# Kernel tuning notes

Hardware: AMD Instinct MI355X
Metric: run time of the kernel (lower is better)

Reference implementation:

```python
import jax, jax.numpy as jnp
import numpy as np

B, S, D = 1, 2048, 2048
HQ, HKV, HD = 32, 8, 64
EXPAND = HQ // HKV

def _rotate_half(x):
    x1, x2 = x[..., : x.shape[-1] // 2], x[..., x.shape[-1] // 2 :]
    return jnp.concatenate((-x2, x1), axis=-1)

def setup_inputs() -> dict:
    key = jax.random.key(0)
    k1, k2, k3 = jax.random.split(key, 3)
    hidden_states = jax.random.normal(k1, (B, S, D), dtype=jnp.float32)
    # Llama weight init scale ~ small
    Wq = jax.random.normal(k2, (HQ * HD, D), dtype=jnp.float32) * 0.02
    Wk = jax.random.normal(k3, (HKV * HD, D), dtype=jnp.float32) * 0.02
    # true rotary cos/sin tables, shape [B, S, HD]
    inv_freq = 1.0 / (10000.0 ** (jnp.arange(0, HD, 2, dtype=jnp.float32) / HD))
    pos = jnp.arange(S, dtype=jnp.float32)
    freqs = pos[:, None] * inv_freq[None, :]            # [S, HD/2]
    emb = jnp.concatenate((freqs, freqs), axis=-1)       # [S, HD]
    cos = jnp.broadcast_to(jnp.cos(emb)[None], (B, S, HD))
    sin = jnp.broadcast_to(jnp.sin(emb)[None], (B, S, HD))
    attn_mask = jnp.zeros((B, 1, S, S), dtype=jnp.float32)  # accepted but unused by the module
    return {"hidden_states": hidden_states, "cos": cos, "sin": sin,
            "attn_mask": attn_mask, "Wq": Wq, "Wk": Wk}

def reference(hidden_states, cos, sin, attn_mask, Wq, Wk):
    b, s, _ = hidden_states.shape
    # projections (nn.Linear, no bias): x @ W.T
    q = hidden_states @ Wq.T                              # [b, s, HQ*HD]
    k = hidden_states @ Wk.T                              # [b, s, HKV*HD]
    q = q.reshape(b, s, HQ, HD).transpose(0, 2, 1, 3)     # [b, HQ, s, HD]
    k = k.reshape(b, s, HKV, HD).transpose(0, 2, 1, 3)    # [b, HKV, s, HD]
    c = cos[:, None, :, :]                                # unsqueeze_dim=1
    sn = sin[:, None, :, :]
    q = q * c + _rotate_half(q) * sn
    k = k * c + _rotate_half(k) * sn
    k = jnp.repeat(k, EXPAND, axis=1)                     # GQA repeat_interleave -> [b, HQ, s, HD]
    scores = jnp.einsum('bhqd,bhkd->bhqk', q, k)          # NO 1/sqrt(d) scaling (faithful)
    return jax.nn.softmax(scores, axis=-1)
```

## Files before the change

kernel.cpp:

```cpp
#include <hip/hip_runtime.h>
#include <hip/hip_bf16.h>

typedef _Float16 half8 __attribute__((ext_vector_type(8)));
typedef float floatx4 __attribute__((ext_vector_type(4)));

#define SEQ 2048
#define DIM 2048
#define HQ 32
#define HKV 8
#define HD 64
#define NQ (HQ*HD)
#define NK (HKV*HD)
#define NTOT (NQ+NK)
#define LOG2E 1.44269504088896340736f

#define GLOAD_LDS16(g, l) \
    __builtin_amdgcn_global_load_lds( \
        (const __attribute__((address_space(1))) void*)(g), \
        (__attribute__((address_space(3))) void*)(l), 16, 0, 0)

__global__ __launch_bounds__(256) void convert_kernel(
    const float* __restrict__ X, const float* __restrict__ Wq,
    const float* __restrict__ Wk, _Float16* __restrict__ Xh,
    _Float16* __restrict__ Wh)
{
    const long c   = (long)blockIdx.x * 256 + threadIdx.x;
    const long nxc = (long)SEQ * DIM / 8;
    const float* src;
    _Float16* dst;
    if (c < nxc) {
        src = X + c * 8;
        dst = Xh + c * 8;
    } else {
        long f = (c - nxc) * 8;
        src = (f < (long)NQ * DIM) ? Wq + f : Wk + (f - (long)NQ * DIM);
        dst = Wh + f;
    }
    float4 a = ((const float4*)src)[0];
    float4 b = ((const float4*)src)[1];
    half8 h = {(_Float16)a.x, (_Float16)a.y, (_Float16)a.z, (_Float16)a.w,
               (_Float16)b.x, (_Float16)b.y, (_Float16)b.z, (_Float16)b.w};
    *(half8*)dst = h;
}

__global__ __launch_bounds__(256) void gemm1_kernel(
    const _Float16* __restrict__ Xh, const _Float16* __restrict__ Wh,
    const float* __restrict__ cosb, const float* __restrict__ sinb,
    _Float16* __restrict__ qout, _Float16* __restrict__ kout)
{
    __shared__ __align__(16) _Float16 lsA[128 * 64];
    __shared__ __align__(16) _Float16 lsB[128 * 64];
    const int tid  = threadIdx.x;
    const int lane = tid & 63;
    const int wv   = tid >> 6;
    const int wm   = wv & 1, wn = wv >> 1;
    const int m    = lane & 15, quad = lane >> 4;
    const int s0   = blockIdx.x * 128;
    const int n0   = blockIdx.y * 128;

    floatx4 acc[4][4];
    #pragma unroll
    for (int i = 0; i < 4; i++)
        #pragma unroll
        for (int j = 0; j < 4; j++)
            acc[i][j] = floatx4{0.f, 0.f, 0.f, 0.f};

    for (int k0 = 0; k0 < DIM; k0 += 64) {
        __syncthreads();
        #pragma unroll
        for (int r = 0; r < 4; r++) {
            int c    = r * 256 + tid;
            int row  = c >> 3;
            int chg  = (c & 7) ^ (row & 7);
            GLOAD_LDS16(Xh + (long)(s0 + row) * DIM + k0 + chg * 8,
                        (char*)lsA + (r * 256 + wv * 64) * 16);
        }
        #pragma unroll
        for (int r = 0; r < 4; r++) {
            int c    = r * 256 + tid;
            int row  = c >> 3;
            int chg  = (c & 7) ^ (row & 7);
            GLOAD_LDS16(Wh + (long)(n0 + row) * DIM + k0 + chg * 8,
                        (char*)lsB + (r * 256 + wv * 64) * 16);
        }
        __syncthreads();

        #pragma unroll
        for (int kk = 0; kk < 2; kk++) {
            half8 aF[4], bF[4];
            const int pc = ((kk << 2) | quad) ^ (m & 7);
            #pragma unroll
            for (int i = 0; i < 4; i++)
                aF[i] = *(const half8*)(lsA + (wm * 64 + i * 16 + m) * 64 + pc * 8);
            #pragma unroll
            for (int j = 0; j < 4; j++)
                bF[j] = *(const half8*)(lsB + (wn * 64 + j * 16 + m) * 64 + pc * 8);
            #pragma unroll
            for (int i = 0; i < 4; i++)
                #pragma unroll
                for (int j = 0; j < 4; j++)
                    acc[i][j] = __builtin_amdgcn_mfma_f32_16x16x32_f16(
                        aF[i], bF[j], acc[i][j], 0, 0, 0);
        }
    }

    #pragma unroll
    for (int i = 0; i < 4; i++) {
        #pragma unroll
        for (int reg = 0; reg < 4; reg++) {
            int s = s0 + wm * 64 + i * 16 + quad * 4 + reg;
            #pragma unroll
            for (int j = 0; j < 4; j++) {
                int col = n0 + wn * 64 + j * 16 + m;
                int d   = j * 16 + m;
                float v = acc[i][j][reg];
                float partner = (j < 2) ? -acc[i][j + 2][reg] : acc[i][j - 2][reg];
                float cs = cosb[s * HD + d];
                float sn = sinb[s * HD + d];
                float o  = v * cs + partner * sn;
                if (col < NQ) {
                    int hq = col >> 6;
                    qout[((long)hq * SEQ + s) * HD + d] = (_Float16)(o * LOG2E);
                } else {
                    int hk = (col - NQ) >> 6;
                    kout[((long)hk * SEQ + s) * HD + d] = (_Float16)o;
                }
            }
        }
    }
}

__global__ __launch_bounds__(512) void attn_kernel(
    const _Float16* __restrict__ qf, const _Float16* __restrict__ kf,
    float* __restrict__ out)
{
    __shared__ float redm[8][16];
    __shared__ float redl[8][16];
    const int tid  = threadIdx.x;
    const int lane = tid & 63;
    const int w    = tid >> 6;
    const int m    = lane & 15, quad = lane >> 4;
    const int qb   = blockIdx.x;
    const int h    = blockIdx.y;
    const int kvh  = h >> 2;
    const int s0   = qb * 16;

    const _Float16* qbase = qf + ((long)h * SEQ + s0) * HD;
    const _Float16* kbase = kf + (long)kvh * SEQ * HD;

    half8 bQ0 = *(const half8*)(qbase + (long)m * HD + quad * 8);
    half8 bQ1 = *(const half8*)(qbase + (long)m * HD + 32 + quad * 8);

    floatx4 acc[16];
    const _Float16* kp = kbase + (long)(w * 256 + m) * HD + quad * 8;
    half8 aK0 = *(const half8*)(kp);
    half8 aK1 = *(const half8*)(kp + 32);
    #pragma unroll
    for (int ct = 0; ct < 16; ct++) {
        half8 nK0, nK1;
        if (ct < 15) {
            const _Float16* np = kbase + (long)(w * 256 + (ct + 1) * 16 + m) * HD + quad * 8;
            nK0 = *(const half8*)(np);
            nK1 = *(const half8*)(np + 32);
        }
        floatx4 a = floatx4{0.f, 0.f, 0.f, 0.f};
        a = __builtin_amdgcn_mfma_f32_16x16x32_f16(aK0, bQ0, a, 0, 0, 0);
        a = __builtin_amdgcn_mfma_f32_16x16x32_f16(aK1, bQ1, a, 0, 0, 0);
        acc[ct] = a;
        aK0 = nK0;
        aK1 = nK1;
    }

    float lm = acc[0][0];
    #pragma unroll
    for (int ct = 0; ct < 16; ct++)
        #pragma unroll
        for (int r = 0; r < 4; r++) lm = fmaxf(lm, acc[ct][r]);
    lm = fmaxf(lm, __shfl_xor(lm, 16));
    lm = fmaxf(lm, __shfl_xor(lm, 32));
    if (quad == 0) redm[w][m] = lm;
    __syncthreads();
    float g = redm[0][m];
    #pragma unroll
    for (int ww = 1; ww < 8; ww++) g = fmaxf(g, redm[ww][m]);

    float ls = 0.f;
    #pragma unroll
    for (int ct = 0; ct < 16; ct++) {
        #pragma unroll
        for (int r = 0; r < 4; r++) {
            float e = exp2f(acc[ct][r] - g);
            acc[ct][r] = e;
            ls += e;
        }
    }
    ls += __shfl_xor(ls, 16);
    ls += __shfl_xor(ls, 32);
    if (quad == 0) redl[w][m] = ls;
    __syncthreads();
    float tot = 0.f;
    #pragma unroll
    for (int ww = 0; ww < 8; ww++) tot += redl[ww][m];
    float inv = 1.0f / tot;

    float* obase = out + ((long)h * SEQ + s0 + m) * SEQ + w * 256 + quad * 4;
    #pragma unroll
    for (int ct = 0; ct < 16; ct++) {
        floatx4 v = acc[ct];
        v[0] *= inv; v[1] *= inv; v[2] *= inv; v[3] *= inv;
        *(floatx4*)(obase + ct * 16) = v;
    }
}

extern "C" void kernel_launch(void* const* d_in, const int* in_sizes, int n_in,
                              void* d_out, int out_size, void* d_ws, size_t ws_size,
                              hipStream_t stream) {
    const float* hidden = (const float*)d_in[0];
    const float* cosb   = (const float*)d_in[1];
    const float* sinb   = (const float*)d_in[2];
    const float* Wq     = (const float*)d_in[4];
    const float* Wk     = (const float*)d_in[5];
    float* out = (float*)d_out;

    char* ws = (char*)d_ws;
    _Float16* Xh = (_Float16*)ws;
    _Float16* Wh = (_Float16*)(ws + 8388608);
    _Float16* qf = (_Float16*)(ws + 8388608 + 10485760);
    _Float16* kf = (_Float16*)(ws + 8388608 + 10485760 + 8388608);

    convert_kernel<<<4608, 256, 0, stream>>>(hidden, Wq, Wk, Xh, Wh);
    gemm1_kernel<<<dim3(16, 20), 256, 0, stream>>>(Xh, Wh, cosb, sinb, qf, kf);
    attn_kernel<<<dim3(128, 32), 512, 0, stream>>>(qf, kf, out);
}
```

Before: 702.3 us.

## Process two query tiles per block and stage output through LDS for coalesced stores

The attention kernel now handles 32 query rows per block instead of 16, so each K fragment load feeds two query groups. The normalized probabilities are transposed through a 128KB swizzled LDS buffer, letting each wave write full contiguous 1KB rows with nontemporal stores instead of scattered 16-byte chunks. The kernel is also given a launch-bounds occupancy hint of 2 blocks. The costs are twice the accumulator registers, an extra barrier, and LDS use that limits how many blocks fit per CU. There is also a possible hazard: lsT reuse for g=1 follows the g=0 reads with no barrier between them, though each wave only touches its own slice.

```diff
diff --git a/kernel.cpp b/kernel.cpp
--- a/kernel.cpp
+++ b/kernel.cpp
@@ -130,12 +130,14 @@
     }
 }
 
-__global__ __launch_bounds__(512) void attn_kernel(
+__global__ __launch_bounds__(512, 2) void attn_kernel(
     const _Float16* __restrict__ qf, const _Float16* __restrict__ kf,
     float* __restrict__ out)
 {
-    __shared__ float redm[8][16];
-    __shared__ float redl[8][16];
+    __shared__ float lsT[8][16][256];
+    float* redm = &lsT[0][0][0];
+    float* redl = redm + 256;
+
     const int tid  = threadIdx.x;
     const int lane = tid & 63;
     const int w    = tid >> 6;
@@ -143,15 +145,19 @@
     const int qb   = blockIdx.x;
     const int h    = blockIdx.y;
     const int kvh  = h >> 2;
-    const int s0   = qb * 16;
+    const int s0   = qb * 32;
 
     const _Float16* qbase = qf + ((long)h * SEQ + s0) * HD;
     const _Float16* kbase = kf + (long)kvh * SEQ * HD;
 
-    half8 bQ0 = *(const half8*)(qbase + (long)m * HD + quad * 8);
-    half8 bQ1 = *(const half8*)(qbase + (long)m * HD + 32 + quad * 8);
-
-    floatx4 acc[16];
+    half8 bQ[2][2];
+    #pragma unroll
+    for (int g = 0; g < 2; g++) {
+        bQ[g][0] = *(const half8*)(qbase + (long)(g * 16 + m) * HD + quad * 8);
+        bQ[g][1] = *(const half8*)(qbase + (long)(g * 16 + m) * HD + 32 + quad * 8);
+    }
+
+    floatx4 acc[2][16];
     const _Float16* kp = kbase + (long)(w * 256 + m) * HD + quad * 8;
     half8 aK0 = *(const half8*)(kp);
     half8 aK1 = *(const half8*)(kp + 32);
@@ -163,52 +169,83 @@
             nK0 = *(const half8*)(np);
             nK1 = *(const half8*)(np + 32);
         }
-        floatx4 a = floatx4{0.f, 0.f, 0.f, 0.f};
-        a = __builtin_amdgcn_mfma_f32_16x16x32_f16(aK0, bQ0, a, 0, 0, 0);
-        a = __builtin_amdgcn_mfma_f32_16x16x32_f16(aK1, bQ1, a, 0, 0, 0);
-        acc[ct] = a;
+        #pragma unroll
+        for (int g = 0; g < 2; g++) {
+            floatx4 a = floatx4{0.f, 0.f, 0.f, 0.f};
+            a = __builtin_amdgcn_mfma_f32_16x16x32_f16(aK0, bQ[g][0], a, 0, 0, 0);
+            a = __builtin_amdgcn_mfma_f32_16x16x32_f16(aK1, bQ[g][1], a, 0, 0, 0);
+            acc[g][ct] = a;
+        }
         aK0 = nK0;
         aK1 = nK1;
     }
 
-    float lm = acc[0][0];
-    #pragma unroll
-    for (int ct = 0; ct < 16; ct++)
-        #pragma unroll
-        for (int r = 0; r < 4; r++) lm = fmaxf(lm, acc[ct][r]);
-    lm = fmaxf(lm, __shfl_xor(lm, 16));
-    lm = fmaxf(lm, __shfl_xor(lm, 32));
-    if (quad == 0) redm[w][m] = lm;
+    float gmax[2];
+    #pragma unroll
+    for (int g = 0; g < 2; g++) {
+        float lm = acc[g][0][0];
+        #pragma unroll
+        for (int ct = 0; ct < 16; ct++)
+            #pragma unroll
+            for (int r = 0; r < 4; r++) lm = fmaxf(lm, acc[g][ct][r]);
+        lm = fmaxf(lm, __shfl_xor(lm, 16));
+        lm = fmaxf(lm, __shfl_xor(lm, 32));
+        if (quad == 0) redm[(g * 8 + w) * 16 + m] = lm;
+    }
     __syncthreads();
-    float g = redm[0][m];
-    #pragma unroll
-    for (int ww = 1; ww < 8; ww++) g = fmaxf(g, redm[ww][m]);
-
-    float ls = 0.f;
-    #pragma unroll
-    for (int ct = 0; ct < 16; ct++) {
-        #pragma unroll
-        for (int r = 0; r < 4; r++) {
-            float e = exp2f(acc[ct][r] - g);
-            acc[ct][r] = e;
-            ls += e;
-        }
-    }
-    ls += __shfl_xor(ls, 16);
-    ls += __shfl_xor(ls, 32);
-    if (quad == 0) redl[w][m] = ls;
+    #pragma unroll
+    for (int g = 0; g < 2; g++) {
+        float gm = redm[(g * 8 + 0) * 16 + m];
+        #pragma unroll
+        for (int ww = 1; ww < 8; ww++)
+            gm = fmaxf(gm, redm[(g * 8 + ww) * 16 + m]);
+        gmax[g] = gm;
+    }
+
+    float inv_[2];
+    #pragma unroll
+    for (int g = 0; g < 2; g++) {
+        float ls = 0.f;
+        #pragma unroll
+        for (int ct = 0; ct < 16; ct++) {
+            #pragma unroll
+            for (int r = 0; r < 4; r++) {
+                float e = exp2f(acc[g][ct][r] - gmax[g]);
+                acc[g][ct][r] = e;
+                ls += e;
+            }
+        }
+        ls += __shfl_xor(ls, 16);
+        ls += __shfl_xor(ls, 32);
+        if (quad == 0) redl[(g * 8 + w) * 16 + m] = ls;
+    }
     __syncthreads();
-    float tot = 0.f;
-    #pragma unroll
-    for (int ww = 0; ww < 8; ww++) tot += redl[ww][m];
-    float inv = 1.0f / tot;
-
-    float* obase = out + ((long)h * SEQ + s0 + m) * SEQ + w * 256 + quad * 4;
-    #pragma unroll
-    for (int ct = 0; ct < 16; ct++) {
-        floatx4 v = acc[ct];
-        v[0] *= inv; v[1] *= inv; v[2] *= inv; v[3] *= inv;
-        *(floatx4*)(obase + ct * 16) = v;
+    #pragma unroll
+    for (int g = 0; g < 2; g++) {
+        float tot = 0.f;
+        #pragma unroll
+        for (int ww = 0; ww < 8; ww++) tot += redl[(g * 8 + ww) * 16 + m];
+        inv_[g] = 1.0f / tot;
+    }
+    __syncthreads();
+
+    #pragma unroll
+    for (int g = 0; g < 2; g++) {
+        #pragma unroll
+        for (int ct = 0; ct < 16; ct++) {
+            floatx4 v = acc[g][ct];
+            v[0] *= inv_[g]; v[1] *= inv_[g]; v[2] *= inv_[g]; v[3] *= inv_[g];
+            int slot = (ct * 4 + quad) ^ m;
+            *(floatx4*)&lsT[w][m][slot * 4] = v;
+        }
+        #pragma unroll
+        for (int r = 0; r < 16; r++) {
+            int slot = lane ^ r;
+            floatx4 v = *(const floatx4*)&lsT[w][r][slot * 4];
+            float* dst = out + ((long)h * SEQ + s0 + g * 16 + r) * SEQ
+                             + w * 256 + lane * 4;
+            __builtin_nontemporal_store(v, (floatx4*)dst);
+        }
     }
 }
 
@@ -230,5 +267,5 @@
 
     convert_kernel<<<4608, 256, 0, stream>>>(hidden, Wq, Wk, Xh, Wh);
     gemm1_kernel<<<dim3(16, 20), 256, 0, stream>>>(Xh, Wh, cosb, sinb, qf, kf);
-    attn_kernel<<<dim3(128, 32), 512, 0, stream>>>(qf, kf, out);
-}
+    attn_kernel<<<dim3(64, 32), 512, 0, stream>>>(qf, kf, out);
+}
```

Result: faster. 677.4 us (-3.5%).
